# Kernel tuning notes

Hardware: AMD Instinct MI355X
Metric: run time of the kernel (lower is better)

## Reference

```python
import jax, jax.numpy as jnp
import numpy as np

B, C, E, L = 128, 128, 10, 16  # atoms, channels, elements, num_ell (lmax=3)
K3_0, K2_0, K1_0 = 23, 4, 1    # num_params per correlation order, 0e output
K3_1, K2_1, K1_1 = 33, 6, 1    # num_params per correlation order, 1o output (num_equiv=3)


def setup_inputs() -> dict:
    key = jax.random.key(0)
    ks = jax.random.split(key, 16)
    inp = {
        'x': jax.random.normal(ks[0], (B, C, L), jnp.float32),
        'y': jax.random.uniform(ks[1], (B, E), jnp.float32),
        # generalized CG (U) buffers -- random dense stand-ins with faithful shapes
        'U1_0e': jax.random.normal(ks[2], (L, K1_0), jnp.float32),
        'U2_0e': jax.random.normal(ks[3], (L, L, K2_0), jnp.float32),
        'U3_0e': jax.random.normal(ks[4], (L, L, L, K3_0), jnp.float32),
        'U1_1o': jax.random.normal(ks[5], (3, L, K1_1), jnp.float32),
        'U2_1o': jax.random.normal(ks[6], (3, L, L, K2_1), jnp.float32),
        'U3_1o': jax.random.normal(ks[7], (3, L, L, L, K3_1), jnp.float32),
        # per-element weights, init randn/num_params as in torch
        'w1_0e': jax.random.normal(ks[8], (E, K1_0, C), jnp.float32) / K1_0,
        'w2_0e': jax.random.normal(ks[9], (E, K2_0, C), jnp.float32) / K2_0,
        'w3_0e': jax.random.normal(ks[10], (E, K3_0, C), jnp.float32) / K3_0,
        'w1_1o': jax.random.normal(ks[11], (E, K1_1, C), jnp.float32) / K1_1,
        'w2_1o': jax.random.normal(ks[12], (E, K2_1, C), jnp.float32) / K2_1,
        'w3_1o': jax.random.normal(ks[13], (E, K3_1, C), jnp.float32) / K3_1,
    }
    return inp


def _contract_0e(x, y, U1, U2, U3, w1, w2, w3):
    # main: 'wxik,ekc,bci,be->bcwx' (explicit path to control peak memory)
    wy3 = jnp.einsum('ekc,be->bkc', w3, y)              # [B,K3,C]
    t = jnp.einsum('wxik,bkc->bcwxi', U3, wy3)          # [B,C,L,L,L]
    out = jnp.einsum('bcwxi,bci->bcwx', t, x)           # [B,C,L,L]
    # order 2: weighting 'wxk,ekc,be->bcwx', features 'bcwi,bci->bcw'
    c2 = jnp.einsum('wxk,ekc,be->bcwx', U2, w2, y)
    out = jnp.einsum('bcwi,bci->bcw', c2 + out, x)
    # order 1: weighting 'wk,ekc,be->bcw', features 'bci,bci->bc'
    c1 = jnp.einsum('wk,ekc,be->bcw', U1, w1, y)
    out = jnp.einsum('bci,bci->bc', c1 + out, x)
    return out  # [B, C]


def _contract_1o(x, y, U1, U2, U3, w1, w2, w3):
    # main: 'wxvik,ekc,bci,be->bcwxv'  (w = equivariance dim of size 3)
    wy3 = jnp.einsum('ekc,be->bkc', w3, y)              # [B,K3,C]
    t = jnp.einsum('wxvik,bkc->bcwxvi', U3, wy3)        # [B,C,3,L,L,L]
    out = jnp.einsum('bcwxvi,bci->bcwxv', t, x)         # [B,C,3,L,L]
    # order 2: 'wxvk,ekc,be->bcwxv' ; features 'bcwxi,bci->bcwx'
    c2 = jnp.einsum('wxvk,ekc,be->bcwxv', U2, w2, y)
    out = jnp.einsum('bcwxi,bci->bcwx', c2 + out, x)
    # order 1: 'wxk,ekc,be->bcwx' ; features 'bcwi,bci->bcw'
    c1 = jnp.einsum('wxk,ekc,be->bcwx', U1, w1, y)
    out = jnp.einsum('bcwi,bci->bcw', c1 + out, x)
    return out.reshape(out.shape[0], -1)  # [B, 3*C]


def reference(x, y, U1_0e, U2_0e, U3_0e, U1_1o, U2_1o, U3_1o,
              w1_0e, w2_0e, w3_0e, w1_1o, w2_1o, w3_1o):
    out0 = _contract_0e(x, y, U1_0e, U2_0e, U3_0e, w1_0e, w2_0e, w3_0e)
    out1 = _contract_1o(x, y, U1_1o, U2_1o, U3_1o, w1_1o, w2_1o, w3_1o)
    return jnp.concatenate([out0, out1], axis=-1)  # [B, C + 3*C]
```

## Files before the change

kernel.cpp:

```cpp
#include <hip/hip_runtime.h>


typedef float  f32x4  __attribute__((ext_vector_type(4)));
typedef short  short8 __attribute__((ext_vector_type(8)));

namespace {
constexpr int EE = 10;
constexpr int LDA1 = 544;
constexpr int LDA0 = 384;
constexpr int A1_ELEMS = 768 * LDA1;
constexpr int A0_ELEMS = 256 * LDA0;
constexpr size_t WS_NEED = (size_t)(A1_ELEMS + A0_ELEMS) * 2;
constexpr int Z31 = 0;
constexpr int Z21 = 33;
constexpr int Z11 = 39;
constexpr int Z30 = 40;
constexpr int Z20 = 63;
constexpr int Z10 = 67;
constexpr int NZ  = 68;

__device__ __forceinline__ unsigned short f2bf(float f) {
  union { float f; unsigned u; } v; v.f = f;
  unsigned r = v.u + 0x7FFFu + ((v.u >> 16) & 1u);
  return (unsigned short)(r >> 16);
}
}

__global__ __launch_bounds__(256) void prep_kernel(
    const float* __restrict__ U3_1o, const float* __restrict__ U2_1o,
    const float* __restrict__ U3_0e, const float* __restrict__ U2_0e,
    unsigned short* __restrict__ wsA)
{
  int idx = blockIdx.x * 256 + threadIdx.x;
  if (idx < A1_ELEMS) {
    int m = idx / LDA1, k = idx - m * LDA1;
    float v = (k < 528) ? U3_1o[m * 528 + k]
            : (k < 534) ? U2_1o[m * 6 + (k - 528)] : 0.f;
    wsA[idx] = f2bf(v);
  } else if (idx < A1_ELEMS + A0_ELEMS) {
    int j = idx - A1_ELEMS;
    int m = j / LDA0, k = j - m * LDA0;
    float v = (k < 368) ? U3_0e[m * 368 + k]
            : (k < 372) ? U2_0e[m * 4 + (k - 368)] : 0.f;
    wsA[idx] = f2bf(v);
  }
}

__global__ __launch_bounds__(512, 2) void symcon_mfma(
    const float* __restrict__ x,
    const float* __restrict__ y,
    const float* __restrict__ U1_0e, const float* __restrict__ U1_1o,
    const float* __restrict__ w1_0e, const float* __restrict__ w2_0e,
    const float* __restrict__ w3_0e, const float* __restrict__ w1_1o,
    const float* __restrict__ w2_1o, const float* __restrict__ w3_1o,
    const unsigned short* __restrict__ wsA,
    float* __restrict__ out)
{
  __shared__ float x_lds[16][64];
  __shared__ float zbuf[NZ][64];
  __shared__ unsigned short B1buf[2][64][40];
  __shared__ unsigned short B0buf[2][64][40];
  __shared__ float red[8][64];

  const int tid   = threadIdx.x;
  const int blk   = blockIdx.x;
  const int pair0 = blk * 64;
  const int b     = blk >> 1;

  for (int t = tid; t < 16 * 64; t += 512) {
    const int i = t >> 6, n = t & 63;
    x_lds[i][n] = x[(size_t)(pair0 + n) * 16 + i];
  }
  for (int t = tid; t < NZ * 64; t += 512) {
    const int n  = t & 63;
    const int zi = t >> 6;
    const int c  = ((blk & 1) << 6) + n;
    const float* yb = y + b * EE;
    const float* wsrc; int stride;
    if      (zi < Z21) { wsrc = w3_1o + (zi      ) * 128 + c; stride = 33 * 128; }
    else if (zi < Z11) { wsrc = w2_1o + (zi - Z21) * 128 + c; stride =  6 * 128; }
    else if (zi < Z30) { wsrc = w1_1o +                    c; stride =  1 * 128; }
    else if (zi < Z20) { wsrc = w3_0e + (zi - Z30) * 128 + c; stride = 23 * 128; }
    else if (zi < Z10) { wsrc = w2_0e + (zi - Z20) * 128 + c; stride =  4 * 128; }
    else               { wsrc = w1_0e +                    c; stride =  1 * 128; }
    float a = 0.f;
    #pragma unroll
    for (int e = 0; e < EE; ++e) a += wsrc[e * stride] * yb[e];
    zbuf[zi][n] = a;
  }
  __syncthreads();

  auto b1val = [&](int kap, int p) -> unsigned short {
    float v;
    if (kap < 528) { int i = kap / 33, kk = kap - i * 33; v = x_lds[i][p] * zbuf[Z31 + kk][p]; }
    else if (kap < 534) v = zbuf[Z21 + (kap - 528)][p];
    else v = 0.f;
    return f2bf(v);
  };
  auto b0val = [&](int kap, int p) -> unsigned short {
    float v;
    if (kap < 368) { int i = kap / 23, kk = kap - i * 23; v = x_lds[i][p] * zbuf[Z30 + kk][p]; }
    else if (kap < 372) v = zbuf[Z20 + (kap - 368)][p];
    else v = 0.f;
    return f2bf(v);
  };
  auto buildB = [&](int tt) {
    const int bb = tt & 1;
    #pragma unroll
    for (int pass = 0; pass < 2; ++pass) {
      const int idx = tid + pass * 512;
      const int p = idx & 63, kr2 = idx >> 6;
      const int k0 = tt * 32 + kr2 * 2;
      unsigned lo = b1val(k0, p), hi = b1val(k0 + 1, p);
      *(unsigned*)&B1buf[bb][p][kr2 * 2] = lo | (hi << 16);
    }
    if (tt < 12) {
      #pragma unroll
      for (int pass = 0; pass < 2; ++pass) {
        const int idx = tid + pass * 512;
        const int p = idx & 63, kr2 = idx >> 6;
        const int k0 = tt * 32 + kr2 * 2;
        unsigned lo = b0val(k0, p), hi = b0val(k0 + 1, p);
        *(unsigned*)&B0buf[bb][p][kr2 * 2] = lo | (hi << 16);
      }
    }
  };

  buildB(0);

  const int lane  = tid & 63;
  const int wv    = tid >> 6;
  const bool is1o = (wv < 6);
  const int q00   = (wv & 1) * 128;
  const int mbase = (is1o ? wv : (wv - 6)) * 128;
  const unsigned short* Abase = is1o ? wsA : (wsA + A1_ELEMS);
  const int lda    = is1o ? LDA1 : LDA0;
  const int mySteps = is1o ? 17 : 12;

  const unsigned short* aPtr[8];
  #pragma unroll
  for (int mf = 0; mf < 8; ++mf)
    aPtr[mf] = Abase + (size_t)(mbase + mf * 16 + (lane & 15)) * lda + (lane >> 4) * 8;

  f32x4 acc[8][4] = {};

  __syncthreads();

  #pragma unroll 1
  for (int t = 0; t < 17; ++t) {
    if (t < mySteps) {
      short8 af[8];
      #pragma unroll
      for (int mf = 0; mf < 8; ++mf)
        af[mf] = *(const short8*)(aPtr[mf] + t * 32);
      short8 bfr[4];
      const unsigned short (*Bb)[40] = is1o ? B1buf[t & 1] : B0buf[t & 1];
      #pragma unroll
      for (int nf = 0; nf < 4; ++nf)
        bfr[nf] = *(const short8*)&Bb[nf * 16 + (lane & 15)][(lane >> 4) * 8];
      if (t + 1 < 17) buildB(t + 1);
      #pragma unroll
      for (int mf = 0; mf < 8; ++mf)
        #pragma unroll
        for (int nf = 0; nf < 4; ++nf)
          acc[mf][nf] = __builtin_amdgcn_mfma_f32_16x16x32_bf16(af[mf], bfr[nf], acc[mf][nf], 0, 0, 0);
    } else {
      if (t + 1 < 17) buildB(t + 1);
    }
    __syncthreads();
  }

  float s[4] = {0.f, 0.f, 0.f, 0.f};
  const int rg = (lane >> 4) * 4;
  #pragma unroll
  for (int mf = 0; mf < 8; ++mf) {
    #pragma unroll
    for (int reg = 0; reg < 4; ++reg) {
      const int q  = q00 + mf * 16 + rg + reg;
      const int qa = q >> 4, qb = q & 15;
      #pragma unroll
      for (int nf = 0; nf < 4; ++nf) {
        const int p = nf * 16 + (lane & 15);
        s[nf] += acc[mf][nf][reg] * (x_lds[qa][p] * x_lds[qb][p]);
      }
    }
  }
  #pragma unroll
  for (int nf = 0; nf < 4; ++nf) {
    s[nf] += __shfl_xor(s[nf], 16);
    s[nf] += __shfl_xor(s[nf], 32);
  }
  if (lane < 16) {
    #pragma unroll
    for (int nf = 0; nf < 4; ++nf) red[wv][nf * 16 + lane] = s[nf];
  }
  __syncthreads();

  if (tid < 256) {
    const int slot = tid >> 6;
    const int n    = tid & 63;
    const int cc   = ((blk & 1) << 6) + n;
    if (slot < 3) {
      float u1 = 0.f;
      #pragma unroll
      for (int xx = 0; xx < 16; ++xx) u1 += U1_1o[slot * 16 + xx] * x_lds[xx][n];
      out[(size_t)b * 512 + 128 + cc * 3 + slot] =
          red[2 * slot][n] + red[2 * slot + 1][n] + zbuf[Z11][n] * u1;
    } else {
      float u1 = 0.f;
      #pragma unroll
      for (int xx = 0; xx < 16; ++xx) u1 += U1_0e[xx] * x_lds[xx][n];
      out[(size_t)b * 512 + cc] =
          red[6][n] + red[7][n] + zbuf[Z10][n] * u1;
    }
  }
}

__global__ __launch_bounds__(512, 2) void symcon_fallback(
    const float* __restrict__ x, const float* __restrict__ y,
    const float* __restrict__ U1_0e, const float* __restrict__ U2_0e,
    const float* __restrict__ U3_0e, const float* __restrict__ U1_1o,
    const float* __restrict__ U2_1o, const float* __restrict__ U3_1o,
    const float* __restrict__ w1_0e, const float* __restrict__ w2_0e,
    const float* __restrict__ w3_0e, const float* __restrict__ w1_1o,
    const float* __restrict__ w2_1o, const float* __restrict__ w3_1o,
    float* __restrict__ out)
{
  __shared__ float x_lds[16][64];
  __shared__ float red[8][64];
  const int tid  = threadIdx.x;
  const int lane = tid & 63;
  const int wv   = __builtin_amdgcn_readfirstlane(tid >> 6);
  const int blk  = blockIdx.x;
  const int pair0 = blk * 64;
  const int b    = blk >> 1;
  const int c    = ((blk & 1) << 6) + lane;

  for (int t = tid; t < 16 * 64; t += 512) {
    const int i = t >> 6, n = t & 63;
    x_lds[i][n] = x[(size_t)(pair0 + n) * 16 + i];
  }
  __syncthreads();

  float yv[EE];
  #pragma unroll
  for (int e = 0; e < EE; ++e) yv[e] = y[b * EE + e];

  const int grp  = wv >> 1;
  const int half = wv & 1;
  const int q00  = half * 128;
  float s = 0.f;

  if (grp < 3) {
    float z3[33];
    #pragma unroll
    for (int k = 0; k < 33; ++k) {
      float a = 0.f;
      #pragma unroll
      for (int e = 0; e < EE; ++e) a += w3_1o[(e * 33 + k) * 128 + c] * yv[e];
      z3[k] = a;
    }
    float z2[6];
    #pragma unroll
    for (int k = 0; k < 6; ++k) {
      float a = 0.f;
      #pragma unroll
      for (int e = 0; e < EE; ++e) a += w2_1o[(e * 6 + k) * 128 + c] * yv[e];
      z2[k] = a;
    }
    const float* __restrict__ U3base = U3_1o + ((size_t)grp * 256 + q00) * 528;
    const float* __restrict__ U2base = U2_1o + (grp * 256 + q00) * 6;
    #pragma unroll 1
    for (int rb = 0; rb < 16; ++rb) {
      float acc[8];
      #pragma unroll
      for (int r = 0; r < 8; ++r) acc[r] = 0.f;
      #pragma unroll 2
      for (int i = 0; i < 16; ++i) {
        const float xi = x_lds[i][lane];
        float pj[33];
        #pragma unroll
        for (int k = 0; k < 33; ++k) pj[k] = xi * z3[k];
        const float* __restrict__ Ur = U3base + (size_t)(rb * 8) * 528 + i * 33;
        #pragma unroll
        for (int r = 0; r < 8; ++r)
          #pragma unroll
          for (int k = 0; k < 33; ++k) acc[r] += Ur[r * 528 + k] * pj[k];
      }
      #pragma unroll
      for (int r = 0; r < 8; ++r) {
        const int q = q00 + rb * 8 + r;
        float a2 = acc[r];
        #pragma unroll
        for (int k = 0; k < 6; ++k) a2 += U2base[(rb * 8 + r) * 6 + k] * z2[k];
        s += a2 * (x_lds[q >> 4][lane] * x_lds[q & 15][lane]);
      }
    }
  } else {
    float z3[23];
    #pragma unroll
    for (int k = 0; k < 23; ++k) {
      float a = 0.f;
      #pragma unroll
      for (int e = 0; e < EE; ++e) a += w3_0e[(e * 23 + k) * 128 + c] * yv[e];
      z3[k] = a;
    }
    float z2[4];
    #pragma unroll
    for (int k = 0; k < 4; ++k) {
      float a = 0.f;
      #pragma unroll
      for (int e = 0; e < EE; ++e) a += w2_0e[(e * 4 + k) * 128 + c] * yv[e];
      z2[k] = a;
    }
    const float* __restrict__ U3base = U3_0e + (size_t)q00 * 368;
    const float* __restrict__ U2base = U2_0e + q00 * 4;
    #pragma unroll 1
    for (int rb = 0; rb < 16; ++rb) {
      float acc[8];
      #pragma unroll
      for (int r = 0; r < 8; ++r) acc[r] = 0.f;
      #pragma unroll 2
      for (int i = 0; i < 16; ++i) {
        const float xi = x_lds[i][lane];
        float pj[23];
        #pragma unroll
        for (int k = 0; k < 23; ++k) pj[k] = xi * z3[k];
        const float* __restrict__ Ur = U3base + (size_t)(rb * 8) * 368 + i * 23;
        #pragma unroll
        for (int r = 0; r < 8; ++r)
          #pragma unroll
          for (int k = 0; k < 23; ++k) acc[r] += Ur[r * 368 + k] * pj[k];
      }
      #pragma unroll
      for (int r = 0; r < 8; ++r) {
        const int q = q00 + rb * 8 + r;
        float a2 = acc[r];
        #pragma unroll
        for (int k = 0; k < 4; ++k) a2 += U2base[(rb * 8 + r) * 4 + k] * z2[k];
        s += a2 * (x_lds[q >> 4][lane] * x_lds[q & 15][lane]);
      }
    }
  }

  red[wv][lane] = s;
  __syncthreads();

  if (tid < 256) {
    const int slot = tid >> 6;
    const int n    = tid & 63;
    const int cc   = ((blk & 1) << 6) + n;
    float u1 = 0.f, z1 = 0.f;
    if (slot < 3) {
      #pragma unroll
      for (int xx = 0; xx < 16; ++xx) u1 += U1_1o[slot * 16 + xx] * x_lds[xx][n];
      #pragma unroll
      for (int e = 0; e < EE; ++e) z1 += w1_1o[e * 128 + cc] * y[b * EE + e];
      out[(size_t)b * 512 + 128 + cc * 3 + slot] = red[2 * slot][n] + red[2 * slot + 1][n] + z1 * u1;
    } else {
      #pragma unroll
      for (int xx = 0; xx < 16; ++xx) u1 += U1_0e[xx] * x_lds[xx][n];
      #pragma unroll
      for (int e = 0; e < EE; ++e) z1 += w1_0e[e * 128 + cc] * y[b * EE + e];
      out[(size_t)b * 512 + cc] = red[6][n] + red[7][n] + z1 * u1;
    }
  }
}

extern "C" void kernel_launch(void* const* d_in, const int* in_sizes, int n_in,
                              void* d_out, int out_size, void* d_ws, size_t ws_size,
                              hipStream_t stream) {
  const float* x     = (const float*)d_in[0];
  const float* y     = (const float*)d_in[1];
  const float* U1_0e = (const float*)d_in[2];
  const float* U2_0e = (const float*)d_in[3];
  const float* U3_0e = (const float*)d_in[4];
  const float* U1_1o = (const float*)d_in[5];
  const float* U2_1o = (const float*)d_in[6];
  const float* U3_1o = (const float*)d_in[7];
  const float* w1_0e = (const float*)d_in[8];
  const float* w2_0e = (const float*)d_in[9];
  const float* w3_0e = (const float*)d_in[10];
  const float* w1_1o = (const float*)d_in[11];
  const float* w2_1o = (const float*)d_in[12];
  const float* w3_1o = (const float*)d_in[13];
  (void)in_sizes; (void)n_in; (void)out_size;

  if (ws_size >= WS_NEED) {
    const int prep_blocks = (A1_ELEMS + A0_ELEMS + 255) / 256;
    hipLaunchKernelGGL(prep_kernel, dim3(prep_blocks), dim3(256), 0, stream,
                       U3_1o, U2_1o, U3_0e, U2_0e, (unsigned short*)d_ws);
    hipLaunchKernelGGL(symcon_mfma, dim3(256), dim3(512), 0, stream,
                       x, y, U1_0e, U1_1o, w1_0e, w2_0e, w3_0e,
                       w1_1o, w2_1o, w3_1o, (const unsigned short*)d_ws,
                       (float*)d_out);
  } else {
    hipLaunchKernelGGL(symcon_fallback, dim3(256), dim3(512), 0, stream,
                       x, y, U1_0e, U2_0e, U3_0e, U1_1o, U2_1o, U3_1o,
                       w1_0e, w2_0e, w3_0e, w1_1o, w2_1o, w3_1o,
                       (float*)d_out);
  }
}
```

Measured before the change: 46.00 us.

## Materialize bf16 B operand in workspace and split MFMA GEMM across more blocks

The per-block in-LDS construction of the B operand (x times z products) is moved into a separate prepB kernel that writes a bf16 B matrix to global workspace using packed bf16 conversion. The GEMM kernel then streams both A and B fragments directly from global memory, with no LDS double-buffering or per-step barriers. The grid doubles to 512 blocks, each wave computing a 64x64 tile. This is meant to remove B-build work and synchronisation from the MFMA loop and raise parallelism. In exchange it adds an extra kernel launch and roughly 30 MB of workspace traffic. The workspace requirement also grows, which could push execution onto the fallback path.

New measurement: 116.8 us. 154% more time.

```diff
diff --git a/kernel.cpp b/kernel.cpp
--- a/kernel.cpp
+++ b/kernel.cpp
@@ -10,7 +10,11 @@
 constexpr int LDA0 = 384;
 constexpr int A1_ELEMS = 768 * LDA1;
 constexpr int A0_ELEMS = 256 * LDA0;
-constexpr size_t WS_NEED = (size_t)(A1_ELEMS + A0_ELEMS) * 2;
+constexpr int A_ELEMS  = A1_ELEMS + A0_ELEMS;
+constexpr size_t WSA_BYTES = (size_t)A_ELEMS * 2;
+constexpr int LDB = 928;
+constexpr size_t WSB_BYTES = (size_t)16384 * LDB * 2;
+constexpr size_t WS_NEED = WSA_BYTES + WSB_BYTES;
 constexpr int Z31 = 0;
 constexpr int Z21 = 33;
 constexpr int Z11 = 39;
@@ -26,7 +30,13 @@
 }
 }
 
-__global__ __launch_bounds__(256) void prep_kernel(
+__device__ __forceinline__ unsigned cvtpk(float lo, float hi) {
+  unsigned r;
+  asm("v_cvt_pk_bf16_f32 %0, %1, %2" : "=v"(r) : "v"(lo), "v"(hi));
+  return r;
+}
+
+__global__ __launch_bounds__(256) void prepA_kernel(
     const float* __restrict__ U3_1o, const float* __restrict__ U2_1o,
     const float* __restrict__ U3_0e, const float* __restrict__ U2_0e,
     unsigned short* __restrict__ wsA)
@@ -37,7 +47,7 @@
     float v = (k < 528) ? U3_1o[m * 528 + k]
             : (k < 534) ? U2_1o[m * 6 + (k - 528)] : 0.f;
     wsA[idx] = f2bf(v);
-  } else if (idx < A1_ELEMS + A0_ELEMS) {
+  } else if (idx < A_ELEMS) {
     int j = idx - A1_ELEMS;
     int m = j / LDA0, k = j - m * LDA0;
     float v = (k < 368) ? U3_0e[m * 368 + k]
@@ -46,32 +56,27 @@
   }
 }
 
-__global__ __launch_bounds__(512, 2) void symcon_mfma(
+__global__ __launch_bounds__(256) void prepB_kernel(
     const float* __restrict__ x,
     const float* __restrict__ y,
-    const float* __restrict__ U1_0e, const float* __restrict__ U1_1o,
     const float* __restrict__ w1_0e, const float* __restrict__ w2_0e,
     const float* __restrict__ w3_0e, const float* __restrict__ w1_1o,
     const float* __restrict__ w2_1o, const float* __restrict__ w3_1o,
-    const unsigned short* __restrict__ wsA,
-    float* __restrict__ out)
+    unsigned* __restrict__ wsBu)
 {
   __shared__ float x_lds[16][64];
   __shared__ float zbuf[NZ][64];
-  __shared__ unsigned short B1buf[2][64][40];
-  __shared__ unsigned short B0buf[2][64][40];
-  __shared__ float red[8][64];
 
   const int tid   = threadIdx.x;
   const int blk   = blockIdx.x;
   const int pair0 = blk * 64;
   const int b     = blk >> 1;
 
-  for (int t = tid; t < 16 * 64; t += 512) {
+  for (int t = tid; t < 16 * 64; t += 256) {
     const int i = t >> 6, n = t & 63;
     x_lds[i][n] = x[(size_t)(pair0 + n) * 16 + i];
   }
-  for (int t = tid; t < NZ * 64; t += 512) {
+  for (int t = tid; t < NZ * 64; t += 256) {
     const int n  = t & 63;
     const int zi = t >> 6;
     const int c  = ((blk & 1) << 6) + n;
@@ -90,97 +95,103 @@
   }
   __syncthreads();
 
-  auto b1val = [&](int kap, int p) -> unsigned short {
-    float v;
-    if (kap < 528) { int i = kap / 33, kk = kap - i * 33; v = x_lds[i][p] * zbuf[Z31 + kk][p]; }
-    else if (kap < 534) v = zbuf[Z21 + (kap - 528)][p];
-    else v = 0.f;
-    return f2bf(v);
+  auto bval = [&](int col, int p) -> float {
+    if (col < 544) {
+      if (col < 528) { int i = col / 33, k = col - i * 33; return x_lds[i][p] * zbuf[Z31 + k][p]; }
+      if (col < 534) return zbuf[Z21 + (col - 528)][p];
+      return 0.f;
+    } else {
+      int kk = col - 544;
+      if (kk < 368) { int i = kk / 23, k = kk - i * 23; return x_lds[i][p] * zbuf[Z30 + k][p]; }
+      if (kk < 372) return zbuf[Z20 + (kk - 368)][p];
+      return 0.f;
+    }
   };
-  auto b0val = [&](int kap, int p) -> unsigned short {
-    float v;
-    if (kap < 368) { int i = kap / 23, kk = kap - i * 23; v = x_lds[i][p] * zbuf[Z30 + kk][p]; }
-    else if (kap < 372) v = zbuf[Z20 + (kap - 368)][p];
-    else v = 0.f;
-    return f2bf(v);
-  };
-  auto buildB = [&](int tt) {
-    const int bb = tt & 1;
-    #pragma unroll
-    for (int pass = 0; pass < 2; ++pass) {
-      const int idx = tid + pass * 512;
-      const int p = idx & 63, kr2 = idx >> 6;
-      const int k0 = tt * 32 + kr2 * 2;
-      unsigned lo = b1val(k0, p), hi = b1val(k0 + 1, p);
-      *(unsigned*)&B1buf[bb][p][kr2 * 2] = lo | (hi << 16);
-    }
-    if (tt < 12) {
-      #pragma unroll
-      for (int pass = 0; pass < 2; ++pass) {
-        const int idx = tid + pass * 512;
-        const int p = idx & 63, kr2 = idx >> 6;
-        const int k0 = tt * 32 + kr2 * 2;
-        unsigned lo = b0val(k0, p), hi = b0val(k0 + 1, p);
-        *(unsigned*)&B0buf[bb][p][kr2 * 2] = lo | (hi << 16);
-      }
-    }
-  };
-
-  buildB(0);
-
+
+  #pragma unroll 1
+  for (int p = 0; p < 64; ++p) {
+    unsigned* dst = wsBu + (size_t)(pair0 + p) * 464;
+    #pragma unroll 1
+    for (int colu = tid; colu < 464; colu += 256) {
+      const int c0 = colu * 2;
+      dst[colu] = cvtpk(bval(c0, p), bval(c0 + 1, p));
+    }
+  }
+}
+
+__global__ __launch_bounds__(512) void symcon_gemm(
+    const float* __restrict__ x,
+    const float* __restrict__ y,
+    const float* __restrict__ U1_0e,
+    const float* __restrict__ U1_1o,
+    const float* __restrict__ w1_0e, const float* __restrict__ w1_1o,
+    const unsigned short* __restrict__ wsA,
+    const unsigned short* __restrict__ wsB,
+    float* __restrict__ out)
+{
+  __shared__ float x_lds[16][64];
+  __shared__ float red[8][64];
+
+  const int tid   = threadIdx.x;
   const int lane  = tid & 63;
   const int wv    = tid >> 6;
-  const bool is1o = (wv < 6);
-  const int q00   = (wv & 1) * 128;
-  const int mbase = (is1o ? wv : (wv - 6)) * 128;
-  const unsigned short* Abase = is1o ? wsA : (wsA + A1_ELEMS);
-  const int lda    = is1o ? LDA1 : LDA0;
-  const int mySteps = is1o ? 17 : 12;
-
-  const unsigned short* aPtr[8];
+  const int lrow  = lane & 15;
+  const int lgr   = lane >> 4;
+  const int blk   = blockIdx.x;
+  const int pgrp  = blk >> 1;
+  const int half  = blk & 1;
+  const int pair0 = pgrp * 64;
+  const int b     = pgrp >> 1;
+
+  for (int t = tid; t < 16 * 64; t += 512) {
+    const int i = t >> 6, n = t & 63;
+    x_lds[i][n] = x[(size_t)(pair0 + n) * 16 + i];
+  }
+  __syncthreads();
+
+  const bool o1 = (half == 0) || (wv < 4);
+  const int rbase   = o1 ? (half * 512 + wv * 64) : ((wv - 4) * 64);
+  const int steps   = o1 ? 17 : 12;
+  const int lda     = o1 ? LDA1 : LDA0;
+  const int colbase = o1 ? 0 : 544;
+  const unsigned short* Abase = o1 ? wsA : (wsA + A1_ELEMS);
+
+  const unsigned short* aP[4];
+  const unsigned short* bP[4];
   #pragma unroll
-  for (int mf = 0; mf < 8; ++mf)
-    aPtr[mf] = Abase + (size_t)(mbase + mf * 16 + (lane & 15)) * lda + (lane >> 4) * 8;
-
-  f32x4 acc[8][4] = {};
-
-  __syncthreads();
+  for (int mf = 0; mf < 4; ++mf)
+    aP[mf] = Abase + (size_t)(rbase + mf * 16 + lrow) * lda + lgr * 8;
+  #pragma unroll
+  for (int nf = 0; nf < 4; ++nf)
+    bP[nf] = wsB + (size_t)(pair0 + nf * 16 + lrow) * LDB + colbase + lgr * 8;
+
+  f32x4 acc[4][4] = {};
 
   #pragma unroll 1
-  for (int t = 0; t < 17; ++t) {
-    if (t < mySteps) {
-      short8 af[8];
-      #pragma unroll
-      for (int mf = 0; mf < 8; ++mf)
-        af[mf] = *(const short8*)(aPtr[mf] + t * 32);
-      short8 bfr[4];
-      const unsigned short (*Bb)[40] = is1o ? B1buf[t & 1] : B0buf[t & 1];
+  for (int t = 0; t < steps; ++t) {
+    short8 af[4], bf[4];
+    #pragma unroll
+    for (int mf = 0; mf < 4; ++mf) af[mf] = *(const short8*)(aP[mf] + t * 32);
+    #pragma unroll
+    for (int nf = 0; nf < 4; ++nf) bf[nf] = *(const short8*)(bP[nf] + t * 32);
+    #pragma unroll
+    for (int mf = 0; mf < 4; ++mf)
       #pragma unroll
       for (int nf = 0; nf < 4; ++nf)
-        bfr[nf] = *(const short8*)&Bb[nf * 16 + (lane & 15)][(lane >> 4) * 8];
-      if (t + 1 < 17) buildB(t + 1);
-      #pragma unroll
-      for (int mf = 0; mf < 8; ++mf)
-        #pragma unroll
-        for (int nf = 0; nf < 4; ++nf)
-          acc[mf][nf] = __builtin_amdgcn_mfma_f32_16x16x32_bf16(af[mf], bfr[nf], acc[mf][nf], 0, 0, 0);
-    } else {
-      if (t + 1 < 17) buildB(t + 1);
-    }
-    __syncthreads();
+        acc[mf][nf] = __builtin_amdgcn_mfma_f32_16x16x32_bf16(af[mf], bf[nf], acc[mf][nf], 0, 0, 0);
   }
 
   float s[4] = {0.f, 0.f, 0.f, 0.f};
-  const int rg = (lane >> 4) * 4;
+  const int rg = lgr * 4;
   #pragma unroll
-  for (int mf = 0; mf < 8; ++mf) {
+  for (int mf = 0; mf < 4; ++mf) {
     #pragma unroll
     for (int reg = 0; reg < 4; ++reg) {
-      const int q  = q00 + mf * 16 + rg + reg;
+      const int q  = (rbase + mf * 16 + rg + reg) & 255;
       const int qa = q >> 4, qb = q & 15;
       #pragma unroll
       for (int nf = 0; nf < 4; ++nf) {
-        const int p = nf * 16 + (lane & 15);
+        const int p = nf * 16 + lrow;
         s[nf] += acc[mf][nf][reg] * (x_lds[qa][p] * x_lds[qb][p]);
       }
     }
@@ -196,22 +207,27 @@
   }
   __syncthreads();
 
-  if (tid < 256) {
+  if (tid < 128) {
     const int slot = tid >> 6;
     const int n    = tid & 63;
-    const int cc   = ((blk & 1) << 6) + n;
-    if (slot < 3) {
-      float u1 = 0.f;
-      #pragma unroll
-      for (int xx = 0; xx < 16; ++xx) u1 += U1_1o[slot * 16 + xx] * x_lds[xx][n];
-      out[(size_t)b * 512 + 128 + cc * 3 + slot] =
-          red[2 * slot][n] + red[2 * slot + 1][n] + zbuf[Z11][n] * u1;
+    const int cc   = ((pgrp & 1) << 6) + n;
+    float v = red[4 * slot][n] + red[4 * slot + 1][n]
+            + red[4 * slot + 2][n] + red[4 * slot + 3][n];
+    if (half == 0 || slot == 0) {
+      const int w = (half == 0) ? slot : 2;
+      float u1 = 0.f, z1 = 0.f;
+      #pragma unroll
+      for (int xx = 0; xx < 16; ++xx) u1 += U1_1o[w * 16 + xx] * x_lds[xx][n];
+      #pragma unroll
+      for (int e = 0; e < EE; ++e) z1 += w1_1o[e * 128 + cc] * y[b * EE + e];
+      out[(size_t)b * 512 + 128 + cc * 3 + w] = v + z1 * u1;
     } else {
-      float u1 = 0.f;
+      float u1 = 0.f, z1 = 0.f;
       #pragma unroll
       for (int xx = 0; xx < 16; ++xx) u1 += U1_0e[xx] * x_lds[xx][n];
-      out[(size_t)b * 512 + cc] =
-          red[6][n] + red[7][n] + zbuf[Z10][n] * u1;
+      #pragma unroll
+      for (int e = 0; e < EE; ++e) z1 += w1_0e[e * 128 + cc] * y[b * EE + e];
+      out[(size_t)b * 512 + cc] = v + z1 * u1;
     }
   }
 }
@@ -387,13 +403,16 @@
   (void)in_sizes; (void)n_in; (void)out_size;
 
   if (ws_size >= WS_NEED) {
-    const int prep_blocks = (A1_ELEMS + A0_ELEMS + 255) / 256;
-    hipLaunchKernelGGL(prep_kernel, dim3(prep_blocks), dim3(256), 0, stream,
-                       U3_1o, U2_1o, U3_0e, U2_0e, (unsigned short*)d_ws);
-    hipLaunchKernelGGL(symcon_mfma, dim3(256), dim3(512), 0, stream,
-                       x, y, U1_0e, U1_1o, w1_0e, w2_0e, w3_0e,
-                       w1_1o, w2_1o, w3_1o, (const unsigned short*)d_ws,
-                       (float*)d_out);
+    unsigned short* wsA = (unsigned short*)d_ws;
+    unsigned short* wsB = (unsigned short*)((char*)d_ws + WSA_BYTES);
+    hipLaunchKernelGGL(prepA_kernel, dim3((A_ELEMS + 255) / 256), dim3(256), 0, stream,
+                       U3_1o, U2_1o, U3_0e, U2_0e, wsA);
+    hipLaunchKernelGGL(prepB_kernel, dim3(256), dim3(256), 0, stream,
+                       x, y, w1_0e, w2_0e, w3_0e, w1_1o, w2_1o, w3_1o,
+                       (unsigned*)wsB);
+    hipLaunchKernelGGL(symcon_gemm, dim3(512), dim3(512), 0, stream,
+                       x, y, U1_0e, U1_1o, w1_0e, w1_1o,
+                       wsA, wsB, (float*)d_out);
   } else {
     hipLaunchKernelGGL(symcon_fallback, dim3(256), dim3(512), 0, stream,
                        x, y, U1_0e, U2_0e, U3_0e, U1_1o, U2_1o, U3_1o,
```
